# Optimization experiments

Hardware: AMD Instinct MI355X
Metric: run time of the kernel (lower is better)

The kernel has to match this reference:

```python
import jax, jax.numpy as jnp
import numpy as np


def setup_inputs() -> dict:
    key = jax.random.key(0)
    k1, k2 = jax.random.split(key)
    B, C, H, W = 64, 64, 32, 32
    ROWS, COLS, O, KH, KW = 28, 28, 128, 5, 5
    x = jax.random.normal(k1, (B, C, H, W), dtype=jnp.float32)
    weight = jax.random.normal(k2, (ROWS, COLS, O, C, KH, KW), dtype=jnp.float32) * 0.05
    return {"x": x, "weight": weight}


def reference(x, weight):
    # Locally-connected conv (unshared weights), stride 1, no padding.
    # output[b,o,i,j] = sum_{c,u,v} x[b,c,i+u,j+v] * weight[i,j,o,c,u,v]
    rows, cols, O, C, kh, kw = weight.shape
    # patches: [B, C, kh, kw, rows, cols] built from kh*kw shifted views (small fixed loop)
    patches = jnp.stack(
        [jnp.stack([x[:, :, u:u + rows, v:v + cols] for v in range(kw)], axis=2)
         for u in range(kh)], axis=2)
    return jnp.einsum('bcuvij,ijocuv->boij', patches, weight)
```

## Files before the change

### kernel.cpp

```cpp
#include <hip/hip_runtime.h>


typedef __attribute__((ext_vector_type(8))) short bf16x8;
typedef __attribute__((ext_vector_type(4))) float f32x4;
typedef unsigned int u32;
typedef unsigned short u16;

__device__ __forceinline__ u16 f2bf(float f) {
    u32 u = __float_as_uint(f);
    u = (u + 0x7fffu + ((u >> 16) & 1u)) >> 16;
    return (u16)u;
}

__global__ __launch_bounds__(256) void pack_x(const float* __restrict__ x,
                                              u16* __restrict__ P) {
    const int blk = blockIdx.x;
    const int g  = blk / 10;
    const int cb = blk - g * 10;
    const int i = g / 28;
    const int j = g - i * 28;
    const int t = threadIdx.x;
    const int b = t >> 2;
    const int q = t & 3;

    const float* xb = x + b * 65536 + i * 32 + j;
    const unsigned kbase = (unsigned)(cb * 160 + q * 40);

    u16 buf[40];
#pragma unroll
    for (unsigned e = 0; e < 40; ++e) {
        unsigned k = kbase + e;
        unsigned c = k / 25u;
        unsigned r = k - c * 25u;
        unsigned u = r / 5u;
        unsigned v = r - u * 5u;
        buf[e] = f2bf(xb[c * 1024 + u * 32 + v]);
    }
    u16* Pr = P + (((size_t)g * 10 + cb) * 64 + b) * 160 + q * 40;
#pragma unroll
    for (int r = 0; r < 5; ++r)
        *(uint4*)(Pr + r * 8) = *(const uint4*)&buf[r * 8];
}

__device__ __forceinline__ void glds16(const void* g, void* l) {
    __builtin_amdgcn_global_load_lds(
        (const __attribute__((address_space(1))) u32*)g,
        (__attribute__((address_space(3))) u32*)l, 16, 0, 0);
}

__global__ __launch_bounds__(256, 3) void lconv_main(const float* __restrict__ wgt,
                                                     const u16* __restrict__ P,
                                                     float* __restrict__ out) {
    constexpr int KC = 160;
    __shared__ u16 As[2][64 * KC];

    const int bx = blockIdx.x;
    const int s  = (bx >> 3) & 1;
    const int bq = (bx & 7) | ((bx >> 4) << 3);
    const int g  = (bq & 7) * 98 + (bq >> 3);

    const int t = threadIdx.x, lane = t & 63, wv = t >> 6;
    const int l15 = lane & 15, quad = lane >> 4;

    const u16*   Pg = P + (size_t)g * 102400;
    const float* wg = wgt + (size_t)g * 204800 + (size_t)(s * 64) * 1600;
    const float* wrow = wg + (size_t)(wv * 16 + l15) * 1600 + quad * 8;

    f32x4 acc[4];
#pragma unroll
    for (int mt = 0; mt < 4; ++mt) acc[mt] = (f32x4)0.f;

    auto stage = [&](int cb, int buf) {
        const char* src = (const char*)(Pg + cb * 10240);
        char* dst = (char*)&As[buf][0];
#pragma unroll
        for (int r = 0; r < 5; ++r) {
            int off = wv * 1024 + r * 4096;
            glds16(src + off + lane * 16, dst + off);
        }
    };

    stage(0, 0);
    __syncthreads();

    for (int cb = 0; cb < 10; ++cb) {
        const float* wc = wrow + cb * 160;
        f32x4 wr[10];
#pragma unroll
        for (int ks = 0; ks < 5; ++ks) {
            wr[2 * ks]     = *(const f32x4*)(wc + ks * 32);
            wr[2 * ks + 1] = *(const f32x4*)(wc + ks * 32 + 4);
        }
        if (cb < 9) stage(cb + 1, (cb + 1) & 1);

        const u16* A = As[cb & 1];
#pragma unroll
        for (int ks = 0; ks < 5; ++ks) {
            f32x4 w0 = wr[2 * ks], w1 = wr[2 * ks + 1];
            bf16x8 bv;
            bv[0] = (short)f2bf(w0[0]); bv[1] = (short)f2bf(w0[1]);
            bv[2] = (short)f2bf(w0[2]); bv[3] = (short)f2bf(w0[3]);
            bv[4] = (short)f2bf(w1[0]); bv[5] = (short)f2bf(w1[1]);
            bv[6] = (short)f2bf(w1[2]); bv[7] = (short)f2bf(w1[3]);
#pragma unroll
            for (int mt = 0; mt < 4; ++mt) {
                bf16x8 av = *(const bf16x8*)&A[(mt * 16 + l15) * KC + ks * 32 + quad * 8];
                acc[mt] = __builtin_amdgcn_mfma_f32_16x16x32_bf16(av, bv, acc[mt], 0, 0, 0);
            }
        }
        if (cb < 9) __syncthreads();
    }

    const int o = s * 64 + wv * 16 + l15;
#pragma unroll
    for (int mt = 0; mt < 4; ++mt)
#pragma unroll
        for (int r = 0; r < 4; ++r) {
            const int b = mt * 16 + quad * 4 + r;
            out[((size_t)b * 128 + o) * 784 + g] = acc[mt][r];
        }
}

__global__ __launch_bounds__(256, 3) void lconv_mfma(
    const float* __restrict__ x,
    const float* __restrict__ wgt,
    float* __restrict__ out)
{
    constexpr int K = 1600, KC = 64, LDK = KC + 8, O = 128, POS = 784;
    __shared__ u16 As[64][LDK];
    const int bx = blockIdx.x;
    const int g = (bx & 7) * 98 + (bx >> 3);
    const int i = g / 28, j = g - i * 28;
    const int t = threadIdx.x, lane = t & 63, wv = t >> 6;
    const int l15 = lane & 15, quad = lane >> 4;
    const float* xbase = x + i * 32 + j;
    const int sb = t >> 2, sk = (t & 3) * 16;
    const float* xrow = xbase + sb * 65536;
    const float* wpos = wgt + (size_t)g * (size_t)(O * K);
    f32x4 acc[4][2];
#pragma unroll
    for (int mt = 0; mt < 4; ++mt)
#pragma unroll
        for (int nt = 0; nt < 2; ++nt) acc[mt][nt] = (f32x4)0.f;
    for (int kb = 0; kb < K; kb += KC) {
        u32 pk[8];
#pragma unroll
        for (int e = 0; e < 16; e += 2) {
            int k0 = kb + sk + e;
            int c0 = k0 / 25, r0 = k0 - 25 * c0, u0 = r0 / 5, v0 = r0 - 5 * u0;
            int k1 = k0 + 1;
            int c1 = k1 / 25, r1 = k1 - 25 * c1, u1 = r1 / 5, v1 = r1 - 5 * u1;
            float f0 = xrow[c0 * 1024 + u0 * 32 + v0];
            float f1 = xrow[c1 * 1024 + u1 * 32 + v1];
            pk[e >> 1] = (u32)f2bf(f0) | ((u32)f2bf(f1) << 16);
        }
        *(uint4*)&As[sb][sk]     = make_uint4(pk[0], pk[1], pk[2], pk[3]);
        *(uint4*)&As[sb][sk + 8] = make_uint4(pk[4], pk[5], pk[6], pk[7]);
        __syncthreads();
#pragma unroll
        for (int kk = 0; kk < 2; ++kk) {
            bf16x8 bfr[2];
#pragma unroll
            for (int nt = 0; nt < 2; ++nt) {
                const int o = wv * 32 + nt * 16 + l15;
                const float* wp = wpos + (size_t)o * K + (kb + kk * 32 + quad * 8);
                f32x4 w0 = *(const f32x4*)wp;
                f32x4 w1 = *(const f32x4*)(wp + 4);
                bf16x8 bv;
                bv[0] = (short)f2bf(w0[0]); bv[1] = (short)f2bf(w0[1]);
                bv[2] = (short)f2bf(w0[2]); bv[3] = (short)f2bf(w0[3]);
                bv[4] = (short)f2bf(w1[0]); bv[5] = (short)f2bf(w1[1]);
                bv[6] = (short)f2bf(w1[2]); bv[7] = (short)f2bf(w1[3]);
                bfr[nt] = bv;
            }
#pragma unroll
            for (int mt = 0; mt < 4; ++mt) {
                bf16x8 av = *(const bf16x8*)&As[mt * 16 + l15][kk * 32 + quad * 8];
#pragma unroll
                for (int nt = 0; nt < 2; ++nt)
                    acc[mt][nt] = __builtin_amdgcn_mfma_f32_16x16x32_bf16(
                        av, bfr[nt], acc[mt][nt], 0, 0, 0);
            }
        }
        __syncthreads();
    }
#pragma unroll
    for (int mt = 0; mt < 4; ++mt)
#pragma unroll
        for (int nt = 0; nt < 2; ++nt) {
            const int o = wv * 32 + nt * 16 + l15;
#pragma unroll
            for (int r = 0; r < 4; ++r) {
                const int b = mt * 16 + quad * 4 + r;
                out[((size_t)b * O + o) * POS + g] = acc[mt][nt][r];
            }
        }
}

extern "C" void kernel_launch(void* const* d_in, const int* in_sizes, int n_in,
                              void* d_out, int out_size, void* d_ws, size_t ws_size,
                              hipStream_t stream) {
    const float* x   = (const float*)d_in[0];
    const float* wgt = (const float*)d_in[1];
    float* out       = (float*)d_out;
    const size_t PBYTES = 784ull * 10 * 64 * 160 * 2;
    if (ws_size >= PBYTES) {
        pack_x<<<7840, 256, 0, stream>>>(x, (u16*)d_ws);
        lconv_main<<<1568, 256, 0, stream>>>(wgt, (const u16*)d_ws, out);
    } else {
        lconv_mfma<<<784, 256, 0, stream>>>(x, wgt, out);
    }
}
```

Before: 1.072 ms.

## Fuse x im2col packing into main MFMA kernel with vectorized row loads

Removes the separate pack_x kernel and its workspace round trip. The main kernel now builds bf16 patch tiles in LDS directly from x. Each thread loads eight contiguous floats per (c,u) row with aligned vector loads, and a compile-time column offset (j&3), dispatched through a switch on four template instantiations, picks the five needed values. This drops one launch and the global write and read of the packed buffer. In exchange, the x loads and conversions now sit on the main kernel's critical path and are no longer done by async global-to-LDS copies.

```diff
diff --git a/kernel.cpp b/kernel.cpp
--- a/kernel.cpp
+++ b/kernel.cpp
@@ -12,75 +12,44 @@
     return (u16)u;
 }
 
-__global__ __launch_bounds__(256) void pack_x(const float* __restrict__ x,
-                                              u16* __restrict__ P) {
-    const int blk = blockIdx.x;
-    const int g  = blk / 10;
-    const int cb = blk - g * 10;
-    const int i = g / 28;
-    const int j = g - i * 28;
-    const int t = threadIdx.x;
-    const int b = t >> 2;
-    const int q = t & 3;
+template<int DJ>
+__device__ __forceinline__ void run_block(const float* __restrict__ xb,
+                                          const float* __restrict__ wrow,
+                                          float* __restrict__ outp,
+                                          u16* As0, u16* As1,
+                                          int tb, int q, int l15, int quad) {
+    constexpr int KC = 160;
 
-    const float* xb = x + b * 65536 + i * 32 + j;
-    const unsigned kbase = (unsigned)(cb * 160 + q * 40);
-
-    u16 buf[40];
+    auto build = [&](int cb, u16* dstbuf) {
+        u16 bu[40];
 #pragma unroll
-    for (unsigned e = 0; e < 40; ++e) {
-        unsigned k = kbase + e;
-        unsigned c = k / 25u;
-        unsigned r = k - c * 25u;
-        unsigned u = r / 5u;
-        unsigned v = r - u * 5u;
-        buf[e] = f2bf(xb[c * 1024 + u * 32 + v]);
-    }
-    u16* Pr = P + (((size_t)g * 10 + cb) * 64 + b) * 160 + q * 40;
+        for (int half = 0; half < 2; ++half) {
+            float fr[4][8];
 #pragma unroll
-    for (int r = 0; r < 5; ++r)
-        *(uint4*)(Pr + r * 8) = *(const uint4*)&buf[r * 8];
-}
-
-__device__ __forceinline__ void glds16(const void* g, void* l) {
-    __builtin_amdgcn_global_load_lds(
-        (const __attribute__((address_space(1))) u32*)g,
-        (__attribute__((address_space(3))) u32*)l, 16, 0, 0);
-}
-
-__global__ __launch_bounds__(256, 3) void lconv_main(const float* __restrict__ wgt,
-                                                     const u16* __restrict__ P,
-                                                     float* __restrict__ out) {
-    constexpr int KC = 160;
-    __shared__ u16 As[2][64 * KC];
-
-    const int bx = blockIdx.x;
-    const int s  = (bx >> 3) & 1;
-    const int bq = (bx & 7) | ((bx >> 4) << 3);
-    const int g  = (bq & 7) * 98 + (bq >> 3);
-
-    const int t = threadIdx.x, lane = t & 63, wv = t >> 6;
-    const int l15 = lane & 15, quad = lane >> 4;
-
-    const u16*   Pg = P + (size_t)g * 102400;
-    const float* wg = wgt + (size_t)g * 204800 + (size_t)(s * 64) * 1600;
-    const float* wrow = wg + (size_t)(wv * 16 + l15) * 1600 + quad * 8;
+            for (int rw = 0; rw < 4; ++rw) {
+                const int R = cb * 32 + q * 8 + half * 4 + rw;
+                const int c = R / 5, u = R - 5 * c;
+                const float* p = xb + c * 1024 + u * 32;
+                *(f32x4*)&fr[rw][0] = *(const f32x4*)(p);
+                *(f32x4*)&fr[rw][4] = *(const f32x4*)(p + 4);
+            }
+#pragma unroll
+            for (int rw = 0; rw < 4; ++rw)
+#pragma unroll
+                for (int v = 0; v < 5; ++v)
+                    bu[(half * 4 + rw) * 5 + v] = f2bf(fr[rw][DJ + v]);
+        }
+        u16* dst = dstbuf + tb * KC + q * 40;
+#pragma unroll
+        for (int r = 0; r < 5; ++r)
+            *(uint4*)(dst + r * 8) = *(const uint4*)&bu[r * 8];
+    };
 
     f32x4 acc[4];
 #pragma unroll
     for (int mt = 0; mt < 4; ++mt) acc[mt] = (f32x4)0.f;
 
-    auto stage = [&](int cb, int buf) {
-        const char* src = (const char*)(Pg + cb * 10240);
-        char* dst = (char*)&As[buf][0];
-#pragma unroll
-        for (int r = 0; r < 5; ++r) {
-            int off = wv * 1024 + r * 4096;
-            glds16(src + off + lane * 16, dst + off);
-        }
-    };
-
-    stage(0, 0);
+    build(0, As0);
     __syncthreads();
 
     for (int cb = 0; cb < 10; ++cb) {
@@ -91,9 +60,9 @@
             wr[2 * ks]     = *(const f32x4*)(wc + ks * 32);
             wr[2 * ks + 1] = *(const f32x4*)(wc + ks * 32 + 4);
         }
-        if (cb < 9) stage(cb + 1, (cb + 1) & 1);
+        if (cb < 9) build(cb + 1, (cb & 1) ? As0 : As1);
 
-        const u16* A = As[cb & 1];
+        const u16* A = (cb & 1) ? As1 : As0;
 #pragma unroll
         for (int ks = 0; ks < 5; ++ks) {
             f32x4 w0 = wr[2 * ks], w1 = wr[2 * ks + 1];
@@ -111,90 +80,43 @@
         if (cb < 9) __syncthreads();
     }
 
-    const int o = s * 64 + wv * 16 + l15;
 #pragma unroll
     for (int mt = 0; mt < 4; ++mt)
 #pragma unroll
         for (int r = 0; r < 4; ++r) {
             const int b = mt * 16 + quad * 4 + r;
-            out[((size_t)b * 128 + o) * 784 + g] = acc[mt][r];
+            outp[(size_t)b * 100352] = acc[mt][r];
         }
 }
 
-__global__ __launch_bounds__(256, 3) void lconv_mfma(
-    const float* __restrict__ x,
-    const float* __restrict__ wgt,
-    float* __restrict__ out)
-{
-    constexpr int K = 1600, KC = 64, LDK = KC + 8, O = 128, POS = 784;
-    __shared__ u16 As[64][LDK];
+__global__ __launch_bounds__(256, 3) void lconv_fused(const float* __restrict__ x,
+                                                      const float* __restrict__ wgt,
+                                                      float* __restrict__ out) {
+    __shared__ u16 As[2][64 * 160];
+
     const int bx = blockIdx.x;
-    const int g = (bx & 7) * 98 + (bx >> 3);
+    const int s  = (bx >> 3) & 1;
+    const int bq = (bx & 7) | ((bx >> 4) << 3);
+    const int g  = (bq & 7) * 98 + (bq >> 3);
     const int i = g / 28, j = g - i * 28;
+    const int j0 = j & ~3;
+
     const int t = threadIdx.x, lane = t & 63, wv = t >> 6;
     const int l15 = lane & 15, quad = lane >> 4;
-    const float* xbase = x + i * 32 + j;
-    const int sb = t >> 2, sk = (t & 3) * 16;
-    const float* xrow = xbase + sb * 65536;
-    const float* wpos = wgt + (size_t)g * (size_t)(O * K);
-    f32x4 acc[4][2];
-#pragma unroll
-    for (int mt = 0; mt < 4; ++mt)
-#pragma unroll
-        for (int nt = 0; nt < 2; ++nt) acc[mt][nt] = (f32x4)0.f;
-    for (int kb = 0; kb < K; kb += KC) {
-        u32 pk[8];
-#pragma unroll
-        for (int e = 0; e < 16; e += 2) {
-            int k0 = kb + sk + e;
-            int c0 = k0 / 25, r0 = k0 - 25 * c0, u0 = r0 / 5, v0 = r0 - 5 * u0;
-            int k1 = k0 + 1;
-            int c1 = k1 / 25, r1 = k1 - 25 * c1, u1 = r1 / 5, v1 = r1 - 5 * u1;
-            float f0 = xrow[c0 * 1024 + u0 * 32 + v0];
-            float f1 = xrow[c1 * 1024 + u1 * 32 + v1];
-            pk[e >> 1] = (u32)f2bf(f0) | ((u32)f2bf(f1) << 16);
-        }
-        *(uint4*)&As[sb][sk]     = make_uint4(pk[0], pk[1], pk[2], pk[3]);
-        *(uint4*)&As[sb][sk + 8] = make_uint4(pk[4], pk[5], pk[6], pk[7]);
-        __syncthreads();
-#pragma unroll
-        for (int kk = 0; kk < 2; ++kk) {
-            bf16x8 bfr[2];
-#pragma unroll
-            for (int nt = 0; nt < 2; ++nt) {
-                const int o = wv * 32 + nt * 16 + l15;
-                const float* wp = wpos + (size_t)o * K + (kb + kk * 32 + quad * 8);
-                f32x4 w0 = *(const f32x4*)wp;
-                f32x4 w1 = *(const f32x4*)(wp + 4);
-                bf16x8 bv;
-                bv[0] = (short)f2bf(w0[0]); bv[1] = (short)f2bf(w0[1]);
-                bv[2] = (short)f2bf(w0[2]); bv[3] = (short)f2bf(w0[3]);
-                bv[4] = (short)f2bf(w1[0]); bv[5] = (short)f2bf(w1[1]);
-                bv[6] = (short)f2bf(w1[2]); bv[7] = (short)f2bf(w1[3]);
-                bfr[nt] = bv;
-            }
-#pragma unroll
-            for (int mt = 0; mt < 4; ++mt) {
-                bf16x8 av = *(const bf16x8*)&As[mt * 16 + l15][kk * 32 + quad * 8];
-#pragma unroll
-                for (int nt = 0; nt < 2; ++nt)
-                    acc[mt][nt] = __builtin_amdgcn_mfma_f32_16x16x32_bf16(
-                        av, bfr[nt], acc[mt][nt], 0, 0, 0);
-            }
-        }
-        __syncthreads();
+    const int tb = t >> 2, q = t & 3;
+
+    const float* xb = x + tb * 65536 + i * 32 + j0;
+    const float* wrow = wgt + (size_t)g * 204800
+                      + (size_t)(s * 64 + wv * 16 + l15) * 1600 + quad * 8;
+    const int o = s * 64 + wv * 16 + l15;
+    float* outp = out + (size_t)o * 784 + g;
+
+    switch (j & 3) {
+        case 0:  run_block<0>(xb, wrow, outp, &As[0][0], &As[1][0], tb, q, l15, quad); break;
+        case 1:  run_block<1>(xb, wrow, outp, &As[0][0], &As[1][0], tb, q, l15, quad); break;
+        case 2:  run_block<2>(xb, wrow, outp, &As[0][0], &As[1][0], tb, q, l15, quad); break;
+        default: run_block<3>(xb, wrow, outp, &As[0][0], &As[1][0], tb, q, l15, quad); break;
     }
-#pragma unroll
-    for (int mt = 0; mt < 4; ++mt)
-#pragma unroll
-        for (int nt = 0; nt < 2; ++nt) {
-            const int o = wv * 32 + nt * 16 + l15;
-#pragma unroll
-            for (int r = 0; r < 4; ++r) {
-                const int b = mt * 16 + quad * 4 + r;
-                out[((size_t)b * O + o) * POS + g] = acc[mt][nt][r];
-            }
-        }
 }
 
 extern "C" void kernel_launch(void* const* d_in, const int* in_sizes, int n_in,
@@ -203,11 +125,6 @@
     const float* x   = (const float*)d_in[0];
     const float* wgt = (const float*)d_in[1];
     float* out       = (float*)d_out;
-    const size_t PBYTES = 784ull * 10 * 64 * 160 * 2;
-    if (ws_size >= PBYTES) {
-        pack_x<<<7840, 256, 0, stream>>>(x, (u16*)d_ws);
-        lconv_main<<<1568, 256, 0, stream>>>(wgt, (const u16*)d_ws, out);
-    } else {
-        lconv_mfma<<<784, 256, 0, stream>>>(x, wgt, out);
-    }
+    (void)d_ws; (void)ws_size;
+    lconv_fused<<<1568, 256, 0, stream>>>(x, wgt, out);
 }
```

New measurement: 1.015 ms. 5.3% less time.
